# Optimization experiments

Hardware: AMD Instinct MI355X
Metric: run time of the kernel (lower is better)

Reference implementation:

```python
import jax, jax.numpy as jnp
import numpy as np

V, D = 8192, 1024   # vocab size, hidden dims
B, T = 32, 128      # batch, sequence length


def setup_inputs() -> dict:
    key = jax.random.key(0)
    ks = jax.random.split(key, 4)
    scale = (2.0 / (V + D)) ** 0.5
    W_ih = jax.random.normal(ks[0], (D, V), jnp.float32) * scale
    W_hh = jnp.eye(D, dtype=jnp.float32) * 0.5 + jax.random.normal(ks[1], (D, D), jnp.float32) * 0.01
    W_ho = jax.random.normal(ks[2], (V, D), jnp.float32) * scale
    idx = jax.random.randint(ks[3], (B, T), 0, V)
    return {
        "idx": idx,
        "h0": jnp.zeros((B, D), jnp.float32),
        "W_ih": W_ih,
        "b_ih": jnp.zeros((D,), jnp.float32),
        "W_hh": W_hh,
        "b_hh": jnp.zeros((D,), jnp.float32),
        "W_ho": W_ho,
        "b_o": jnp.zeros((V,), jnp.float32),
    }


def reference(idx, h0, W_ih, b_ih, W_hh, b_hh, W_ho, b_o):
    # W_ih @ one_hot(idx) is exactly a column gather of W_ih -> row gather of W_ih.T
    emb = W_ih.T            # [V, D]
    toks = idx.T            # [T, B], scan over time

    def step(h, tok):
        # h: [B, D], tok: [B]
        x_proj = emb[tok]                                        # [B, D]
        h_next = jnp.tanh(x_proj + b_ih + h @ W_hh.T + b_hh)     # [B, D]
        logits = h_next @ W_ho.T + b_o                           # [B, V]
        return h_next, jax.nn.log_softmax(logits, axis=-1)

    _, log_probs = jax.lax.scan(step, h0, toks)  # log_probs: [T, B, V]
    return log_probs
```

## Files before the change

### kernel.cpp

```cpp
#include <hip/hip_runtime.h>
#include <hip/hip_bf16.h>
#include <cstdint>
#include <cstddef>

#define V_ 8192
#define D_ 1024
#define B_ 32
#define T_ 128
#define NBLK 16
#define SENT 0x7FC0u

typedef __attribute__((ext_vector_type(8))) short bf16x8;
typedef __attribute__((ext_vector_type(4))) float f32x4;

__device__ __forceinline__ short f2bf(float f) {
  union { float f; unsigned u; } v; v.f = f;
  unsigned r = v.u + 0x7fffu + ((v.u >> 16) & 1u);
  return (short)(r >> 16);
}

__device__ __forceinline__ float bf2f(unsigned short u) {
  union { unsigned u; float f; } c; c.u = ((unsigned)u) << 16;
  return c.f;
}

__device__ __forceinline__ float fast_tanh(float x) {
  float t = __builtin_amdgcn_exp2f(x * 2.8853900817779268f);
  return 1.0f - 2.0f * __builtin_amdgcn_rcpf(t + 1.0f);
}

__device__ __forceinline__ void lds_load16(const void* g, void* l) {
  __builtin_amdgcn_global_load_lds(
      (const __attribute__((address_space(1))) unsigned int*)g,
      (__attribute__((address_space(3))) unsigned int*)l,
      16, 0, 0);
}

union U4 { int4 i4; unsigned u[4]; unsigned long long q[2]; bf16x8 v; };

__device__ __forceinline__ void load_frag_sc0(const short* ap, U4* out) {
  asm volatile(
      "global_load_dwordx4 %0, %4, off sc0\n\t"
      "global_load_dwordx4 %1, %4, off offset:64 sc0\n\t"
      "global_load_dwordx4 %2, %4, off offset:128 sc0\n\t"
      "global_load_dwordx4 %3, %4, off offset:192 sc0\n\t"
      "s_waitcnt vmcnt(0)"
      : "=&v"(out[0].i4), "=&v"(out[1].i4), "=&v"(out[2].i4), "=&v"(out[3].i4)
      : "v"(ap) : "memory");
}

__global__ __launch_bounds__(256) void conv_bf16_k(const float* __restrict__ in,
                                                   short* __restrict__ out, int n4) {
  int i = blockIdx.x * 256 + threadIdx.x;
  if (i >= n4) return;
  float4 v = reinterpret_cast<const float4*>(in)[i];
  short4 o;
  o.x = f2bf(v.x); o.y = f2bf(v.y); o.z = f2bf(v.z); o.w = f2bf(v.w);
  reinterpret_cast<short4*>(out)[i] = o;
}

__global__ __launch_bounds__(256) void conv_whh(const float* __restrict__ W,
                                                short* __restrict__ Rb,
                                                float* __restrict__ Wdiag) {
  int i = blockIdx.x * 256 + threadIdx.x;
  int n = i >> 10;
  int k = i & (D_ - 1);
  float w = W[i];
  Rb[i] = f2bf(k == n ? 0.0f : w);
  if (k == n) Wdiag[n] = w;
}

__global__ __launch_bounds__(256) void prep_h(const float* __restrict__ h0,
                                              const int* __restrict__ idx,
                                              short* __restrict__ Af,
                                              unsigned* __restrict__ flags,
                                              int* __restrict__ idxT) {
  int i = blockIdx.x * 256 + threadIdx.x;
  __hip_atomic_store((unsigned long long*)(Af + B_ * D_) + i,
                     0x7FC07FC07FC07FC0ull, __ATOMIC_RELAXED, __HIP_MEMORY_SCOPE_AGENT);
  if (i < (B_ * D_) / 2) {
    unsigned lo = (unsigned short)f2bf(h0[2 * i]);
    unsigned hi = (unsigned short)f2bf(h0[2 * i + 1]);
    __hip_atomic_store((unsigned*)Af + i, lo | (hi << 16),
                       __ATOMIC_RELAXED, __HIP_MEMORY_SCOPE_AGENT);
  }
  if (i < 64)
    __hip_atomic_store(flags + i, 0u, __ATOMIC_RELAXED, __HIP_MEMORY_SCOPE_AGENT);
  if (i < T_ * B_) {
    int b = i & (B_ - 1);
    int t = i >> 5;
    idxT[i] = idx[b * T_ + t];
  }
}

__global__ __launch_bounds__(256) void wtrans(const float* __restrict__ W,
                                              const float* __restrict__ b_ih,
                                              const float* __restrict__ b_hh,
                                              short* __restrict__ Wtb) {
  __shared__ float tile[32][33];
  const int tx = threadIdx.x & 31;
  const int ty = threadIdx.x >> 5;
  const int v0 = blockIdx.x * 32;
  const int d0 = blockIdx.y * 32;
#pragma unroll
  for (int i = 0; i < 32; i += 8)
    tile[ty + i][tx] = W[(size_t)(d0 + ty + i) * V_ + v0 + tx];
  __syncthreads();
  const int d = d0 + tx;
  const float bias = b_ih[d] + b_hh[d];
#pragma unroll
  for (int i = 0; i < 32; i += 8)
    Wtb[(size_t)(v0 + ty + i) * D_ + d] = f2bf(tile[tx][ty + i] + bias);
}

__global__ __launch_bounds__(512) void rnn_all(const short* __restrict__ Rb,
                                               const float* __restrict__ Wdiag,
                                               const float* __restrict__ h0,
                                               const short* __restrict__ Wtb,
                                               const int* __restrict__ idxT,
                                               short* __restrict__ Af,
                                               unsigned* __restrict__ flags) {
  __shared__ f32x4 part[8][2][4][64];
  __shared__ int sblk;
  const int tid = threadIdx.x;

  if (tid == 0) {
    unsigned xcc;
    asm volatile("s_getreg_b32 %0, hwreg(HW_REG_XCC_ID)" : "=s"(xcc));
    xcc &= 7u;
    unsigned* cnt = flags + 16;
    unsigned* winner = flags + 24;
    unsigned rank = __hip_atomic_fetch_add(&cnt[xcc], 1u, __ATOMIC_RELAXED,
                                           __HIP_MEMORY_SCOPE_AGENT);
    int my = -1;
    if (rank == 15u) {
      unsigned exp = 0u;
      __hip_atomic_compare_exchange_strong(winner, &exp, xcc + 1u,
                                           __ATOMIC_RELAXED, __ATOMIC_RELAXED,
                                           __HIP_MEMORY_SCOPE_AGENT);
    }
    if (rank < 16u) {
      unsigned wv;
      while ((wv = __hip_atomic_load(winner, __ATOMIC_RELAXED,
                                     __HIP_MEMORY_SCOPE_AGENT)) == 0u)
        __builtin_amdgcn_s_sleep(8);
      if (wv == xcc + 1u) my = (int)rank;
    }
    sblk = my;
  }
  __syncthreads();
  const int blk = sblk;
  if (blk < 0) return;

  __builtin_amdgcn_fence(__ATOMIC_ACQUIRE, "agent");
  if (tid == 0) {
    __hip_atomic_fetch_add(flags + 25, 1u, __ATOMIC_RELAXED, __HIP_MEMORY_SCOPE_AGENT);
    while (__hip_atomic_load(flags + 25, __ATOMIC_RELAXED,
                             __HIP_MEMORY_SCOPE_AGENT) < 16u)
      __builtin_amdgcn_s_sleep(1);
  }
  __syncthreads();

  const int lane = tid & 63;
  const int w = tid >> 6;
  const int n0 = blk * 64;
  const int fcol = lane & 15;
  const int l16 = lane >> 4;
  const int ks = w * 128;

  bf16x8 bfrag[4][4];
#pragma unroll
  for (int ni = 0; ni < 4; ++ni) {
    const short* bp = Rb + (size_t)(n0 + ni * 16 + fcol) * D_ + ks + l16 * 8;
#pragma unroll
    for (int kk = 0; kk < 4; ++kk)
      bfrag[ni][kk] = *reinterpret_cast<const bf16x8*>(bp + kk * 32);
  }

  const int mi_e = w >> 2;
  const int ni_e = w & 3;
  const int n_e = n0 + ni_e * 16 + fcol;
  const int mbase = mi_e * 16 + l16 * 4;
  const float wd = Wdiag[n_e];
  float hf[4];
#pragma unroll
  for (int q = 0; q < 4; ++q)
    hf[q] = h0[(size_t)(mbase + q) * D_ + n_e];

  float xv[4];
  {
    int4 tk = *reinterpret_cast<const int4*>(idxT + mbase);
    xv[0] = bf2f(*(const unsigned short*)(Wtb + (size_t)tk.x * D_ + n_e));
    xv[1] = bf2f(*(const unsigned short*)(Wtb + (size_t)tk.y * D_ + n_e));
    xv[2] = bf2f(*(const unsigned short*)(Wtb + (size_t)tk.z * D_ + n_e));
    xv[3] = bf2f(*(const unsigned short*)(Wtb + (size_t)tk.w * D_ + n_e));
  }

  for (int t = 0; t < T_; ++t) {
    const size_t slot = (size_t)t * (B_ * D_);
    const short* fp0 = Af + slot + (size_t)fcol * D_ + ks + l16 * 8;
    const short* fp1 = fp0 + 16 * D_;
    U4 a[8];
    {
      int bud = 0;
      while (true) {
        load_frag_sc0(fp0, a);
        load_frag_sc0(fp1, a + 4);
        unsigned bad = 0u;
#pragma unroll
        for (int i = 0; i < 8; ++i)
#pragma unroll
          for (int j = 0; j < 4; ++j) {
            unsigned d = a[i].u[j];
            bad |= ((d & 0xFFFFu) == SENT) | ((d >> 16) == SENT);
          }
        if (!__any((int)bad)) break;
        if (++bud >= 256) {
          bud = 0;
          __builtin_amdgcn_fence(__ATOMIC_ACQUIRE, "agent");
        }
      }
    }
    bf16x8 af[2][4];
#pragma unroll
    for (int mi = 0; mi < 2; ++mi)
#pragma unroll
      for (int kk = 0; kk < 4; ++kk)
        af[mi][kk] = a[mi * 4 + kk].v;

#pragma unroll
    for (int mi = 0; mi < 2; ++mi)
#pragma unroll
      for (int ni = 0; ni < 4; ++ni) {
        f32x4 acc = {0.f, 0.f, 0.f, 0.f};
#pragma unroll
        for (int kk = 0; kk < 4; ++kk)
          acc = __builtin_amdgcn_mfma_f32_16x16x32_bf16(af[mi][kk], bfrag[ni][kk], acc, 0, 0, 0);
        part[w][mi][ni][lane] = acc;
      }
    __syncthreads();

    f32x4 s = part[0][mi_e][ni_e][lane];
#pragma unroll
    for (int r = 1; r < 8; ++r) s += part[r][mi_e][ni_e][lane];

    const size_t nslot = (size_t)(t + 1) * (B_ * D_);
#pragma unroll
    for (int q2 = 0; q2 < 4; ++q2) {
      float v = fast_tanh(xv[q2] + s[q2] + hf[q2] * wd);
      hf[q2] = v;
      unsigned ov = (unsigned)(unsigned short)f2bf(v);
      short* pf = Af + nslot + (size_t)(mbase + q2) * D_ + n_e;
      asm volatile("global_store_short %0, %1, off sc0" :: "v"(pf), "v"(ov) : "memory");
    }

    if (t < T_ - 1) {
      int4 tk = *reinterpret_cast<const int4*>(idxT + (t + 1) * B_ + mbase);
      xv[0] = bf2f(*(const unsigned short*)(Wtb + (size_t)tk.x * D_ + n_e));
      xv[1] = bf2f(*(const unsigned short*)(Wtb + (size_t)tk.y * D_ + n_e));
      xv[2] = bf2f(*(const unsigned short*)(Wtb + (size_t)tk.z * D_ + n_e));
      xv[3] = bf2f(*(const unsigned short*)(Wtb + (size_t)tk.w * D_ + n_e));
    }

    asm volatile("s_waitcnt vmcnt(0)" ::: "memory");
    __syncthreads();
  }
}

__global__ __launch_bounds__(256) void gemm_logits(const short* __restrict__ A,
                                                   const short* __restrict__ Bt,
                                                   const float* __restrict__ b_o,
                                                   short* __restrict__ Cb) {
  constexpr int K = D_;
  __shared__ __align__(16) short As[128 * 64];
  __shared__ __align__(16) short Bs[128 * 64];

  const int tid = threadIdx.x;
  const int lane = tid & 63;
  const int w = tid >> 6;
  const int wr = w >> 1, wc = w & 1;
  const int bid = blockIdx.y * 64 + blockIdx.x;
  const int swz = (bid & 7) * 256 + (bid >> 3);
  const int r0 = (swz >> 6) * 128;
  const int c0 = (swz & 63) * 128;

  f32x4 acc[4][4] = {};

  for (int k0 = 0; k0 < K; k0 += 64) {
#pragma unroll
    for (int i = 0; i < 4; ++i) {
      int c = tid + 256 * i;
      int cb = (tid & ~63) + 256 * i;
      int row = c >> 3;
      int colc = ((c & 7) ^ (row & 7)) * 8;
      lds_load16(A + (size_t)(r0 + row) * K + k0 + colc, &As[cb * 8]);
      lds_load16(Bt + (size_t)(c0 + row) * K + k0 + colc, &Bs[cb * 8]);
    }
    asm volatile("s_waitcnt vmcnt(0)" ::: "memory");
    __syncthreads();

#pragma unroll
    for (int kk = 0; kk < 2; ++kk) {
      bf16x8 af[4], bfr[4];
      const int fcol = lane & 15;
      const int chunk = (kk * 4 + (lane >> 4)) ^ (fcol & 7);
#pragma unroll
      for (int i = 0; i < 4; ++i)
        af[i] = *reinterpret_cast<const bf16x8*>(&As[(wr * 64 + i * 16 + fcol) * 64 + chunk * 8]);
#pragma unroll
      for (int j = 0; j < 4; ++j)
        bfr[j] = *reinterpret_cast<const bf16x8*>(&Bs[(wc * 64 + j * 16 + fcol) * 64 + chunk * 8]);
#pragma unroll
      for (int i = 0; i < 4; ++i)
#pragma unroll
        for (int j = 0; j < 4; ++j)
          acc[i][j] = __builtin_amdgcn_mfma_f32_16x16x32_bf16(af[i], bfr[j], acc[i][j], 0, 0, 0);
    }
    __syncthreads();
  }

  const int fcol = lane & 15;
  const int frow = (lane >> 4) * 4;
#pragma unroll
  for (int i = 0; i < 4; ++i) {
    int row = r0 + wr * 64 + i * 16 + frow;
#pragma unroll
    for (int j = 0; j < 4; ++j) {
      int col = c0 + wc * 64 + j * 16 + fcol;
      float bias = b_o[col];
#pragma unroll
      for (int q = 0; q < 4; ++q)
        Cb[(size_t)(row + q) * 16384 + col] = f2bf(acc[i][j][q] + bias);
    }
  }
}

__global__ __launch_bounds__(256) void logsoftmax(float* __restrict__ out) {
  __shared__ float red[4];
  __shared__ float red2[4];
  const short* row = (const short*)out + (size_t)blockIdx.x * 16384;
  float* orow = out + (size_t)blockIdx.x * V_;
  const int tid = threadIdx.x;

  float v[32];
  float mx = -1e30f;
#pragma unroll
  for (int i = 0; i < 4; ++i) {
    uint4 pk = reinterpret_cast<const uint4*>(row)[i * 256 + tid];
    unsigned uu[4] = {pk.x, pk.y, pk.z, pk.w};
#pragma unroll
    for (int j = 0; j < 4; ++j) {
      float lo = bf2f((unsigned short)(uu[j] & 0xFFFFu));
      float hi = bf2f((unsigned short)(uu[j] >> 16));
      v[i * 8 + 2 * j] = lo;
      v[i * 8 + 2 * j + 1] = hi;
      mx = fmaxf(mx, fmaxf(lo, hi));
    }
  }
#pragma unroll
  for (int off = 32; off > 0; off >>= 1) mx = fmaxf(mx, __shfl_xor(mx, off, 64));
  if ((tid & 63) == 0) red[tid >> 6] = mx;
  __syncthreads();
  mx = fmaxf(fmaxf(red[0], red[1]), fmaxf(red[2], red[3]));

  float sum = 0.f;
#pragma unroll
  for (int k = 0; k < 32; ++k) sum += expf(v[k] - mx);
#pragma unroll
  for (int off = 32; off > 0; off >>= 1) sum += __shfl_xor(sum, off, 64);
  if ((tid & 63) == 0) red2[tid >> 6] = sum;
  __syncthreads();
  sum = (red2[0] + red2[1]) + (red2[2] + red2[3]);

  const float lse = mx + logf(sum);
#pragma unroll
  for (int i = 0; i < 4; ++i) {
    float4 w1 = {v[i * 8 + 0] - lse, v[i * 8 + 1] - lse, v[i * 8 + 2] - lse, v[i * 8 + 3] - lse};
    float4 w2 = {v[i * 8 + 4] - lse, v[i * 8 + 5] - lse, v[i * 8 + 6] - lse, v[i * 8 + 7] - lse};
    *reinterpret_cast<float4*>(&orow[(i * 256 + tid) * 8]) = w1;
    *reinterpret_cast<float4*>(&orow[(i * 256 + tid) * 8 + 4]) = w2;
  }
}

extern "C" void kernel_launch(void* const* d_in, const int* in_sizes, int n_in,
                              void* d_out, int out_size, void* d_ws, size_t ws_size,
                              hipStream_t stream) {
  const int* idx = (const int*)d_in[0];
  const float* h0 = (const float*)d_in[1];
  const float* W_ih = (const float*)d_in[2];
  const float* b_ih = (const float*)d_in[3];
  const float* W_hh = (const float*)d_in[4];
  const float* b_hh = (const float*)d_in[5];
  const float* W_ho = (const float*)d_in[6];
  const float* b_o = (const float*)d_in[7];
  float* out = (float*)d_out;

  char* ws = (char*)d_ws;
  short* Wb = (short*)(ws + 8454144);
  short* Rb = (short*)(ws + 25231360);
  float* Wdiag = (float*)(ws + 27328512);
  short* Wtb = (short*)(ws + 27332608);
  unsigned* flags = (unsigned*)(ws + 44109824);
  int* idxT = (int*)(ws + 44113920);
  short* Af = (short*)(ws + 44130304);

  conv_bf16_k<<<dim3(8192), dim3(256), 0, stream>>>(W_ho, Wb, (V_ * D_) / 4);
  conv_whh<<<dim3(4096), dim3(256), 0, stream>>>(W_hh, Rb, Wdiag);
  prep_h<<<dim3(4096), dim3(256), 0, stream>>>(h0, idx, Af, flags, idxT);
  wtrans<<<dim3(V_ / 32, D_ / 32), dim3(256), 0, stream>>>(W_ih, b_ih, b_hh, Wtb);

  rnn_all<<<dim3(256), dim3(512), 0, stream>>>(Rb, Wdiag, h0, Wtb, idxT, Af, flags);

  gemm_logits<<<dim3(V_ / 128, (T_ * B_) / 128), dim3(256), 0, stream>>>(
      Af + B_ * D_, Wb, b_o, (short*)out);
  logsoftmax<<<dim3(T_ * B_), dim3(256), 0, stream>>>(out);
}
```

Measured before the change: 667.0 us.

## Overlap W_ho bf16 conversion with RNN recurrence using idle blocks; merge prep kernels

The 240 blocks of the persistent RNN kernel that lose the XCC election, and used to exit, now pull chunks of W_ho through an atomic counter and convert them to bf16. This hides the weight conversion behind the serial recurrence instead of running it as a separate kernel. The W_hh conversion and h/flags/index prep kernels are merged into one launch, and the block-index swizzle in the logits GEMM is removed. The helper blocks compete with the 16 recurrence blocks for memory bandwidth, and the plain GEMM tile order may reduce L2 reuse.

```diff
diff --git a/kernel.cpp b/kernel.cpp
--- a/kernel.cpp
+++ b/kernel.cpp
@@ -49,33 +49,22 @@
       : "v"(ap) : "memory");
 }
 
-__global__ __launch_bounds__(256) void conv_bf16_k(const float* __restrict__ in,
-                                                   short* __restrict__ out, int n4) {
+__global__ __launch_bounds__(256) void prep2(const float* __restrict__ W,
+                                             const float* __restrict__ h0,
+                                             const int* __restrict__ idx,
+                                             short* __restrict__ Rb,
+                                             float* __restrict__ Wdiag,
+                                             short* __restrict__ Af,
+                                             unsigned* __restrict__ flags,
+                                             int* __restrict__ idxT) {
   int i = blockIdx.x * 256 + threadIdx.x;
-  if (i >= n4) return;
-  float4 v = reinterpret_cast<const float4*>(in)[i];
-  short4 o;
-  o.x = f2bf(v.x); o.y = f2bf(v.y); o.z = f2bf(v.z); o.w = f2bf(v.w);
-  reinterpret_cast<short4*>(out)[i] = o;
-}
-
-__global__ __launch_bounds__(256) void conv_whh(const float* __restrict__ W,
-                                                short* __restrict__ Rb,
-                                                float* __restrict__ Wdiag) {
-  int i = blockIdx.x * 256 + threadIdx.x;
-  int n = i >> 10;
-  int k = i & (D_ - 1);
-  float w = W[i];
-  Rb[i] = f2bf(k == n ? 0.0f : w);
-  if (k == n) Wdiag[n] = w;
-}
-
-__global__ __launch_bounds__(256) void prep_h(const float* __restrict__ h0,
-                                              const int* __restrict__ idx,
-                                              short* __restrict__ Af,
-                                              unsigned* __restrict__ flags,
-                                              int* __restrict__ idxT) {
-  int i = blockIdx.x * 256 + threadIdx.x;
+  {
+    int n = i >> 10;
+    int k = i & (D_ - 1);
+    float w = W[i];
+    Rb[i] = f2bf(k == n ? 0.0f : w);
+    if (k == n) Wdiag[n] = w;
+  }
   __hip_atomic_store((unsigned long long*)(Af + B_ * D_) + i,
                      0x7FC07FC07FC07FC0ull, __ATOMIC_RELAXED, __HIP_MEMORY_SCOPE_AGENT);
   if (i < (B_ * D_) / 2) {
@@ -119,9 +108,12 @@
                                                const short* __restrict__ Wtb,
                                                const int* __restrict__ idxT,
                                                short* __restrict__ Af,
-                                               unsigned* __restrict__ flags) {
+                                               unsigned* __restrict__ flags,
+                                               const float* __restrict__ W_ho,
+                                               short* __restrict__ Wb) {
   __shared__ f32x4 part[8][2][4][64];
   __shared__ int sblk;
+  __shared__ unsigned schunk;
   const int tid = threadIdx.x;
 
   if (tid == 0) {
@@ -150,7 +142,26 @@
   }
   __syncthreads();
   const int blk = sblk;
-  if (blk < 0) return;
+
+  if (blk < 0) {
+    while (true) {
+      if (tid == 0)
+        schunk = __hip_atomic_fetch_add(flags + 26, 1u, __ATOMIC_RELAXED,
+                                        __HIP_MEMORY_SCOPE_AGENT);
+      __syncthreads();
+      unsigned c = schunk;
+      __syncthreads();
+      if (c >= 1024u) return;
+#pragma unroll
+      for (int r = 0; r < 4; ++r) {
+        int i = (int)c * 2048 + r * 512 + tid;
+        float4 v = reinterpret_cast<const float4*>(W_ho)[i];
+        short4 o;
+        o.x = f2bf(v.x); o.y = f2bf(v.y); o.z = f2bf(v.z); o.w = f2bf(v.w);
+        reinterpret_cast<short4*>(Wb)[i] = o;
+      }
+    }
+  }
 
   __builtin_amdgcn_fence(__ATOMIC_ACQUIRE, "agent");
   if (tid == 0) {
@@ -279,10 +290,8 @@
   const int lane = tid & 63;
   const int w = tid >> 6;
   const int wr = w >> 1, wc = w & 1;
-  const int bid = blockIdx.y * 64 + blockIdx.x;
-  const int swz = (bid & 7) * 256 + (bid >> 3);
-  const int r0 = (swz >> 6) * 128;
-  const int c0 = (swz & 63) * 128;
+  const int r0 = blockIdx.y * 128;
+  const int c0 = blockIdx.x * 128;
 
   f32x4 acc[4][4] = {};
 
@@ -404,12 +413,11 @@
   int* idxT = (int*)(ws + 44113920);
   short* Af = (short*)(ws + 44130304);
 
-  conv_bf16_k<<<dim3(8192), dim3(256), 0, stream>>>(W_ho, Wb, (V_ * D_) / 4);
-  conv_whh<<<dim3(4096), dim3(256), 0, stream>>>(W_hh, Rb, Wdiag);
-  prep_h<<<dim3(4096), dim3(256), 0, stream>>>(h0, idx, Af, flags, idxT);
+  prep2<<<dim3(4096), dim3(256), 0, stream>>>(W_hh, h0, idx, Rb, Wdiag, Af, flags, idxT);
   wtrans<<<dim3(V_ / 32, D_ / 32), dim3(256), 0, stream>>>(W_ih, b_ih, b_hh, Wtb);
 
-  rnn_all<<<dim3(256), dim3(512), 0, stream>>>(Rb, Wdiag, h0, Wtb, idxT, Af, flags);
+  rnn_all<<<dim3(256), dim3(512), 0, stream>>>(Rb, Wdiag, h0, Wtb, idxT, Af, flags,
+                                               W_ho, Wb);
 
   gemm_logits<<<dim3(V_ / 128, (T_ * B_) / 128), dim3(256), 0, stream>>>(
       Af + B_ * D_, Wb, b_o, (short*)out);
```

After: 666.1 us. Within noise of the previous version (-0.1%).
